# Optimization experiments

Hardware: AMD Instinct MI355X
Metric: run time of the kernel (lower is better)

## Reference

```python
import jax, jax.numpy as jnp
import numpy as np

D = 256; NH = 8; NL = 4; NP = 4; HD = D // NH
LEVELS = ((80, 80), (40, 40), (20, 20), (10, 10))
B = 8; LTXT = 32
LVIS = sum(h * w for h, w in LEVELS)  # 8500


def layer_norm(x, g, b):
    m = x.mean(-1, keepdims=True)
    v = ((x - m) ** 2).mean(-1, keepdims=True)
    return (x - m) * jax.lax.rsqrt(v + 1e-5) * g + b


def gelu(x):
    return jax.nn.gelu(x, approximate=False)


def sample_level(v, H, W, loc):
    # v: [B,NH,H*W,HD] level value; loc: [B,Lq,NH,NP,2] normalized [0,1] (x,y)
    # bilinear, align_corners=False, zero padding (matches grid_sample in MSDeformAttn)
    x = loc[..., 0] * W - 0.5
    y = loc[..., 1] * H - 0.5
    x0 = jnp.floor(x); y0 = jnp.floor(y)
    fx = x - x0; fy = y - y0
    Bq, Lq = loc.shape[0], loc.shape[1]
    out = jnp.zeros((Bq, NH, Lq * NP, HD), v.dtype)
    for dx in (0, 1):
        for dy in (0, 1):
            xi = x0 + dx; yi = y0 + dy
            w = (fx if dx else 1.0 - fx) * (fy if dy else 1.0 - fy)
            valid = (xi >= 0) & (xi < W) & (yi >= 0) & (yi < H)
            xi_c = jnp.clip(xi, 0, W - 1).astype(jnp.int32)
            yi_c = jnp.clip(yi, 0, H - 1).astype(jnp.int32)
            idx = (yi_c * W + xi_c).transpose(0, 2, 1, 3).reshape(Bq, NH, Lq * NP)
            wv = jnp.where(valid, w, 0.0).transpose(0, 2, 1, 3).reshape(Bq, NH, Lq * NP, 1)
            g = jnp.take_along_axis(v, idx[..., None], axis=2)  # [B,NH,Lq*NP,HD]
            out = out + g * wv
    return out.reshape(Bq, NH, Lq, NP, HD)


def setup_inputs() -> dict:
    key = jax.random.key(0)
    ks = iter(jax.random.split(key, 64))
    def rn(shape, s=1.0):
        return jax.random.normal(next(ks), shape, jnp.float32) * s
    inp = {}
    inp['txt_tokens'] = rn((B, LTXT, D))
    inp['vis_tokens'] = rn((B, LVIS, D))
    for i, (H, W) in enumerate(LEVELS):
        inp[f'feat{i}'] = rn((B, D, H, W))
    inp['spatial_shapes'] = jnp.array(LEVELS, jnp.int32)
    starts = np.cumsum([0] + [h * w for h, w in LEVELS])[:NL]
    inp['level_start_index'] = jnp.array(starts, jnp.int32)
    inp['reference_points'] = jax.random.uniform(next(ks), (B, LTXT, NL, 2), jnp.float32)
    inp['txt_pos'] = rn((B, LTXT, D), 0.02)
    inp['vis_pos'] = rn((B, LVIS, D), 0.02)
    s = 0.02
    # MSDeformAttn params
    inp['W_off'] = rn((D, NH * NL * NP * 2), s); inp['b_off'] = rn((NH * NL * NP * 2,), s)
    inp['W_aw'] = rn((D, NH * NL * NP), s); inp['b_aw'] = rn((NH * NL * NP,), s)
    inp['W_v'] = rn((D, D), s); inp['b_v'] = rn((D,), s)
    inp['W_do'] = rn((D, D), s); inp['b_do'] = rn((D,), s)
    # adapter projections
    inp['W_q_lvi'] = rn((D, D), s); inp['b_q_lvi'] = rn((D,), s)
    inp['W_out_lvi'] = rn((D, D), s); inp['b_out_lvi'] = rn((D,), s)
    # lvi norms + ffn
    inp['ln1_g'] = jnp.ones((D,)); inp['ln1_b'] = jnp.zeros((D,))
    inp['ln2_g'] = jnp.ones((D,)); inp['ln2_b'] = jnp.zeros((D,))
    inp['ffn1_W1'] = rn((D, 4 * D), s); inp['ffn1_b1'] = rn((4 * D,), s)
    inp['ffn1_W2'] = rn((4 * D, D), s); inp['ffn1_b2'] = rn((D,), s)
    # vli MultiheadAttention
    inp['Wq_m'] = rn((D, D), s); inp['bq_m'] = rn((D,), s)
    inp['Wk_m'] = rn((D, D), s); inp['bk_m'] = rn((D,), s)
    inp['Wv_m'] = rn((D, D), s); inp['bv_m'] = rn((D,), s)
    inp['Wo_m'] = rn((D, D), s); inp['bo_m'] = rn((D,), s)
    inp['vln1_g'] = jnp.ones((D,)); inp['vln1_b'] = jnp.zeros((D,))
    inp['vln2_g'] = jnp.ones((D,)); inp['vln2_b'] = jnp.zeros((D,))
    inp['ffn2_W1'] = rn((D, 4 * D), s); inp['ffn2_b1'] = rn((4 * D,), s)
    inp['ffn2_W2'] = rn((4 * D, D), s); inp['ffn2_b2'] = rn((D,), s)
    return inp


def reference(txt_tokens, vis_tokens, feat0, feat1, feat2, feat3, reference_points, txt_pos, vis_pos,
              W_off, b_off, W_aw, b_aw, W_v, b_v, W_do, b_do,
              W_q_lvi, b_q_lvi, W_out_lvi, b_out_lvi,
              ln1_g, ln1_b, ln2_g, ln2_b,
              ffn1_W1, ffn1_b1, ffn1_W2, ffn1_b2,
              Wq_m, bq_m, Wk_m, bk_m, Wv_m, bv_m, Wo_m, bo_m,
              vln1_g, vln1_b, vln2_g, vln2_b,
              ffn2_W1, ffn2_b1, ffn2_W2, ffn2_b2,
              spatial_shapes, level_start_index):
    # ---- lvi: deformable multi-scale attention (txt queries sample vis features) ----
    txt_query = txt_tokens + txt_pos
    q = txt_query @ W_q_lvi + b_q_lvi
    feats = (feat0, feat1, feat2, feat3)
    value = jnp.concatenate([f.reshape(f.shape[0], D, -1).transpose(0, 2, 1) for f in feats], axis=1)
    v = (value @ W_v + b_v).reshape(B, LVIS, NH, HD)
    off = (q @ W_off + b_off).reshape(B, LTXT, NH, NL, NP, 2)
    aw = jax.nn.softmax((q @ W_aw + b_aw).reshape(B, LTXT, NH, NL * NP), axis=-1).reshape(B, LTXT, NH, NL, NP)
    normalizer = jnp.array([[w, h] for h, w in LEVELS], jnp.float32)  # (W,H) per level
    loc = reference_points[:, :, None, :, None, :] + off / normalizer[None, None, None, :, None, :]
    acc = jnp.zeros((B, NH, LTXT, HD), v.dtype)
    start = 0
    for l, (H, W) in enumerate(LEVELS):
        vl = v[:, start:start + H * W].transpose(0, 2, 1, 3)  # [B,NH,HW,HD]
        s = sample_level(vl, H, W, loc[:, :, :, l])           # [B,NH,Lq,NP,HD]
        awl = aw[:, :, :, l].transpose(0, 2, 1, 3)[..., None]  # [B,NH,Lq,NP,1]
        acc = acc + (s * awl).sum(3)
        start += H * W
    d_out = acc.transpose(0, 2, 1, 3).reshape(B, LTXT, D) @ W_do + b_do
    txt_attn = d_out @ W_out_lvi + b_out_lvi
    txt_res = layer_norm(txt_tokens + txt_attn, ln1_g, ln1_b)
    ff = gelu(txt_res @ ffn1_W1 + ffn1_b1) @ ffn1_W2 + ffn1_b2
    txt_res = layer_norm(txt_res + ff, ln2_g, ln2_b)
    # ---- vli: standard cross attention (vis queries attend txt) ----
    vis_query = vis_tokens + vis_pos
    vis_key = txt_res + txt_pos
    qh = (vis_query @ Wq_m + bq_m).reshape(B, LVIS, NH, HD)
    kh = (vis_key @ Wk_m + bk_m).reshape(B, LTXT, NH, HD)
    vh = (vis_key @ Wv_m + bv_m).reshape(B, LTXT, NH, HD)
    scores = jnp.einsum('bqhd,bkhd->bhqk', qh, kh) / np.float32(np.sqrt(HD))
    p = jax.nn.softmax(scores, axis=-1)
    mo = jnp.einsum('bhqk,bkhd->bqhd', p, vh).reshape(B, LVIS, D) @ Wo_m + bo_m
    vis_res = layer_norm(vis_tokens + mo, vln1_g, vln1_b)
    ff2 = gelu(vis_res @ ffn2_W1 + ffn2_b1) @ ffn2_W2 + ffn2_b2
    vis_res = layer_norm(vis_res + ff2, vln2_g, vln2_b)
    attn_weights = p.mean(axis=1)  # torch MHA averages over heads
    return (txt_res, vis_res, attn_weights)
```

## Files before the change

### kernel.cpp

```cpp
#include <hip/hip_runtime.h>
#include <cstddef>

#define DD   256
#define NHH  8
#define HDD  32
#define BB   8
#define LT   32
#define LV   8500

typedef unsigned short u16;
typedef unsigned int   u32;
typedef __attribute__((ext_vector_type(8))) short short8;
typedef __attribute__((ext_vector_type(8))) unsigned short ushort8;
typedef __attribute__((ext_vector_type(4))) float f32x4;

__device__ __forceinline__ float gelu_f(float x) {
  return 0.5f * x * (1.0f + erff(x * 0.70710678118654752440f));
}

__device__ __forceinline__ u16 f2bf(float x) {
  u32 u = __float_as_uint(x);
  u += 0x7FFFu + ((u >> 16) & 1u);
  return (u16)(u >> 16);
}
__device__ __forceinline__ float bf2f(u16 h) { return __uint_as_float((u32)h << 16); }

__device__ __forceinline__ void gload16(const u16* g, u16* l) {
  __builtin_amdgcn_global_load_lds(
      (const __attribute__((address_space(1))) void*)g,
      (__attribute__((address_space(3))) void*)l, 16, 0, 0);
}

enum { AM_PLAIN = 0, AM_ADD = 1, AM_FEAT = 2, AM_HI = 3, AM_SPLIT = 4 };
enum { EP_BIAS = 0, EP_GELU = 1, EP_ACC = 2 };

template<int BM, int BN, int TM, int TN, int AMODE, int EPI>
__launch_bounds__(256)
__global__ void gemm_k(const float* __restrict__ A0, const float* __restrict__ A1,
                       const float* __restrict__ Wt, const float* __restrict__ bias,
                       float* __restrict__ C, int M, int K, int ldw, int ldc)
{
  constexpr int BK = 16;
  __shared__ __align__(16) float As[BK][BM];
  __shared__ __align__(16) float Ws[BK][BN];
  const int tid  = threadIdx.x;
  const int row0 = blockIdx.x * BM;
  const int col0 = blockIdx.y * BN;
  const int tx = tid % (BN / TN);
  const int ty = tid / (BN / TN);
  float acc[TM][TN] = {};

  for (int k0 = 0; k0 < K; k0 += BK) {
    {
      constexpr int AU = BM * BK / 4;
      for (int u = tid; u < AU; u += 256) {
        int m  = u / (BK / 4);
        int kq = (u % (BK / 4)) * 4;
        int grow = row0 + m;
        float4 v = make_float4(0.f, 0.f, 0.f, 0.f);
        if (grow < M) {
          v = *(const float4*)(A0 + (size_t)grow * K + k0 + kq);
          if constexpr (AMODE == AM_ADD) {
            float4 w = *(const float4*)(A1 + (size_t)grow * K + k0 + kq);
            v.x += w.x; v.y += w.y; v.z += w.z; v.w += w.w;
          }
        }
        As[kq + 0][m] = v.x; As[kq + 1][m] = v.y;
        As[kq + 2][m] = v.z; As[kq + 3][m] = v.w;
      }
    }
    {
      constexpr int WU = BK * BN / 4;
      for (int u = tid; u < WU; u += 256) {
        int k  = u / (BN / 4);
        int n4 = (u % (BN / 4)) * 4;
        *(float4*)&Ws[k][n4] =
            *(const float4*)(Wt + (size_t)(k0 + k) * ldw + col0 + n4);
      }
    }
    __syncthreads();

    #pragma unroll
    for (int k = 0; k < BK; ++k) {
      float a[TM], bv[TN];
      #pragma unroll
      for (int i = 0; i < TM; ++i) a[i] = As[k][ty * TM + i];
      #pragma unroll
      for (int j = 0; j < TN; j += 4) {
        float4 t4 = *(const float4*)&Ws[k][tx * TN + j];
        bv[j] = t4.x; bv[j + 1] = t4.y; bv[j + 2] = t4.z; bv[j + 3] = t4.w;
      }
      #pragma unroll
      for (int i = 0; i < TM; ++i)
        #pragma unroll
        for (int j = 0; j < TN; ++j)
          acc[i][j] = fmaf(a[i], bv[j], acc[i][j]);
    }
    __syncthreads();
  }

  #pragma unroll
  for (int i = 0; i < TM; ++i) {
    int r = row0 + ty * TM + i;
    if (r >= M) continue;
    #pragma unroll
    for (int j4 = 0; j4 < TN; j4 += 4) {
      int c = col0 + tx * TN + j4;
      float4 v = make_float4(acc[i][j4], acc[i][j4 + 1], acc[i][j4 + 2], acc[i][j4 + 3]);
      float4 b4 = *(const float4*)(bias + c);
      v.x += b4.x; v.y += b4.y; v.z += b4.z; v.w += b4.w;
      if constexpr (EPI == EP_GELU) {
        v.x = gelu_f(v.x); v.y = gelu_f(v.y); v.z = gelu_f(v.z); v.w = gelu_f(v.w);
      }
      *(float4*)(C + (size_t)r * ldc + c) = v;
    }
  }
}

__global__ void wsplit_kernel(const float* __restrict__ W, u16* __restrict__ hi,
                              u16* __restrict__ lo, int total, int Nw)
{
  int id = blockIdx.x * 256 + threadIdx.x;
  if (id >= total) return;
  int k = id / Nw, n = id - k * Nw;
  float x = W[id];
  u16 h = f2bf(x);
  u16 l = f2bf(x - bf2f(h));
  int o = ((k >> 3) * Nw + n) * 8 + (k & 7);
  hi[o] = h; lo[o] = l;
}

template<int AMODE, int EPI>
__global__ __launch_bounds__(256) void mgemm(
    const void* __restrict__ Ap, const void* __restrict__ A1p,
    const u16* __restrict__ Whi, const u16* __restrict__ Wlo,
    const float* __restrict__ bias, void* __restrict__ Cp,
    int M, int K, int lda, int ldc, int Nw, int wcol0, int ks0,
    const float* __restrict__ f0, const float* __restrict__ f1,
    const float* __restrict__ f2, const float* __restrict__ f3)
{
  constexpr bool GL = (AMODE >= 3);
  constexpr int SMEM_U16 = GL ? (AMODE == AM_SPLIT ? 16384 : 8192) : 8256;
  __shared__ __align__(16) u16 smem[SMEM_U16];
  const int tid  = threadIdx.x;
  const int lane = tid & 63;
  const int w    = tid >> 6;
  const int wr   = w >> 1, wc = w & 1;
  const int row0  = blockIdx.x * 128;
  const int colC0 = blockIdx.y * 128;
  f32x4 acc[4][4] = {};
  const int nk = K >> 5;

  if constexpr (GL) {
    const u16* Ah = (const u16*)Ap;
    const u16* Al = (const u16*)A1p;
    auto stage = [&](int t, int buf) {
      #pragma unroll
      for (int p = 0; p < 2; ++p) {
        int i = w + p * 4;
        int r = row0 + i * 16 + (lane >> 2);
        if (r >= M) r = M - 1;
        size_t goff = (size_t)r * lda + t * 32 + (lane & 3) * 8;
        gload16(Ah + goff, &smem[buf * 4096 + i * 512]);
        if constexpr (AMODE == AM_SPLIT)
          gload16(Al + goff, &smem[8192 + buf * 4096 + i * 512]);
      }
    };
    stage(0, 0);
    __syncthreads();
    for (int kt = 0; kt < nk; ++kt) {
      const int cur = kt & 1;
      if (kt + 1 < nk) stage(kt + 1, cur ^ 1);
      const int slot = lane >> 4;
      const int lrow = lane & 15;
      short8 ah[4], al[4], bh[4], bl[4];
      #pragma unroll
      for (int m = 0; m < 4; ++m) {
        int off = cur * 4096 + (((wr * 64 + m * 16 + lrow) << 2) + slot) * 8;
        ah[m] = *(const short8*)&smem[off];
        if constexpr (AMODE == AM_SPLIT) al[m] = *(const short8*)&smem[8192 + off];
      }
      #pragma unroll
      for (int n = 0; n < 4; ++n) {
        size_t off = ((size_t)((ks0 + kt) * 4 + slot) * Nw + wcol0 + colC0 + wc * 64 + n * 16 + lrow) * 8;
        bh[n] = *(const short8*)(Whi + off);
        bl[n] = *(const short8*)(Wlo + off);
      }
      #pragma unroll
      for (int m = 0; m < 4; ++m)
        #pragma unroll
        for (int n = 0; n < 4; ++n) {
          acc[m][n] = __builtin_amdgcn_mfma_f32_16x16x32_bf16(ah[m], bh[n], acc[m][n], 0, 0, 0);
          acc[m][n] = __builtin_amdgcn_mfma_f32_16x16x32_bf16(ah[m], bl[n], acc[m][n], 0, 0, 0);
          if constexpr (AMODE == AM_SPLIT)
            acc[m][n] = __builtin_amdgcn_mfma_f32_16x16x32_bf16(al[m], bh[n], acc[m][n], 0, 0, 0);
        }
      __syncthreads();
    }
  } else {
    u16* Ahi = smem;
    u16* Alo = smem + 4128;
    for (int kt = 0; kt < nk; ++kt) {
      #pragma unroll
      for (int p = 0; p < 4; ++p) {
        int j = tid + p * 256;
        int row, f4;
        if constexpr (AMODE == AM_FEAT) { f4 = j >> 7; row = j & 127; }
        else                            { row = j >> 3; f4 = j & 7; }
        int gr = row0 + row;
        float4 v = make_float4(0.f, 0.f, 0.f, 0.f);
        if (gr < M) {
          if constexpr (AMODE == AM_FEAT) {
            int b = gr / LV;
            int s = gr - b * LV;
            int l = (s >= 8400) ? 3 : (s >= 8000) ? 2 : (s >= 6400) ? 1 : 0;
            const float* fp = (l == 0) ? f0 : (l == 1) ? f1 : (l == 2) ? f2 : f3;
            const int hw = (l == 0) ? 6400 : (l == 1) ? 1600 : (l == 2) ? 400 : 100;
            const int st = (l == 0) ? 0 : (l == 1) ? 6400 : (l == 2) ? 8000 : 8400;
            const float* base = fp + ((size_t)b * DD + (kt * 32 + f4 * 4)) * hw + (s - st);
            v.x = base[0];
            v.y = base[(size_t)hw];
            v.z = base[2 * (size_t)hw];
            v.w = base[3 * (size_t)hw];
          } else {
            const float* Af = (const float*)Ap;
            v = *(const float4*)(Af + (size_t)gr * lda + kt * 32 + f4 * 4);
            if constexpr (AMODE == AM_ADD) {
              float4 u2 = *(const float4*)((const float*)A1p + (size_t)gr * lda + kt * 32 + f4 * 4);
              v.x += u2.x; v.y += u2.y; v.z += u2.z; v.w += u2.w;
            }
          }
        }
        int slot = f4 >> 1, half = f4 & 1;
        int off = (slot * 129 + row) * 8 + half * 4;
        u16 h0 = f2bf(v.x), h1 = f2bf(v.y), h2 = f2bf(v.z), h3 = f2bf(v.w);
        uint2 hp; hp.x = (u32)h0 | ((u32)h1 << 16); hp.y = (u32)h2 | ((u32)h3 << 16);
        *(uint2*)&Ahi[off] = hp;
        u16 l0 = f2bf(v.x - bf2f(h0)), l1 = f2bf(v.y - bf2f(h1));
        u16 l2 = f2bf(v.z - bf2f(h2)), l3 = f2bf(v.w - bf2f(h3));
        uint2 lp; lp.x = (u32)l0 | ((u32)l1 << 16); lp.y = (u32)l2 | ((u32)l3 << 16);
        *(uint2*)&Alo[off] = lp;
      }
      __syncthreads();

      const int slot = lane >> 4;
      const int lrow = lane & 15;
      short8 ah[4], al[4], bh[4], bl[4];
      #pragma unroll
      for (int m = 0; m < 4; ++m) {
        int off = (slot * 129 + wr * 64 + m * 16 + lrow) * 8;
        ah[m] = *(const short8*)&Ahi[off];
        al[m] = *(const short8*)&Alo[off];
      }
      #pragma unroll
      for (int n = 0; n < 4; ++n) {
        size_t off = ((size_t)((ks0 + kt) * 4 + slot) * Nw + wcol0 + colC0 + wc * 64 + n * 16 + lrow) * 8;
        bh[n] = *(const short8*)(Whi + off);
        bl[n] = *(const short8*)(Wlo + off);
      }
      #pragma unroll
      for (int m = 0; m < 4; ++m)
        #pragma unroll
        for (int n = 0; n < 4; ++n) {
          acc[m][n] = __builtin_amdgcn_mfma_f32_16x16x32_bf16(ah[m], bh[n], acc[m][n], 0, 0, 0);
          acc[m][n] = __builtin_amdgcn_mfma_f32_16x16x32_bf16(ah[m], bl[n], acc[m][n], 0, 0, 0);
          acc[m][n] = __builtin_amdgcn_mfma_f32_16x16x32_bf16(al[m], bh[n], acc[m][n], 0, 0, 0);
        }
      __syncthreads();
    }
  }

  const int lrow = lane & 15;
  #pragma unroll
  for (int m = 0; m < 4; ++m) {
    #pragma unroll
    for (int j = 0; j < 4; ++j) {
      int r = row0 + wr * 64 + m * 16 + ((lane >> 4) << 2) + j;
      if (r >= M) continue;
      #pragma unroll
      for (int n = 0; n < 4; ++n) {
        int c = colC0 + wc * 64 + n * 16 + lrow;
        float v = acc[m][n][j];
        if constexpr (EPI == EP_BIAS) {
          ((float*)Cp)[(size_t)r * ldc + c] = v + bias[c];
        } else if constexpr (EPI == EP_GELU) {
          ((u16*)Cp)[(size_t)r * ldc + c] = f2bf(gelu_f(v + bias[c]));
        } else {
          ((float*)Cp)[(size_t)r * ldc + c] += v;
        }
      }
    }
  }
}

__device__ __forceinline__ float4 ln_core(float4 x, const float* g, const float* bta, int lane) {
  float s  = x.x + x.y + x.z + x.w;
  float s2 = x.x * x.x + x.y * x.y + x.z * x.z + x.w * x.w;
  #pragma unroll
  for (int m = 1; m < 64; m <<= 1) {
    s  += __shfl_xor(s, m);
    s2 += __shfl_xor(s2, m);
  }
  float mean = s * (1.0f / 256.0f);
  float var  = s2 * (1.0f / 256.0f) - mean * mean;
  float rstd = rsqrtf(var + 1e-5f);
  float4 gg = *(const float4*)(g + lane * 4);
  float4 bb = *(const float4*)(bta + lane * 4);
  float4 o;
  o.x = (x.x - mean) * rstd * gg.x + bb.x;
  o.y = (x.y - mean) * rstd * gg.y + bb.y;
  o.z = (x.z - mean) * rstd * gg.z + bb.z;
  o.w = (x.w - mean) * rstd * gg.w + bb.w;
  return o;
}

__global__ void ln_kernel(const float* __restrict__ X, const float* __restrict__ R,
                          const float* __restrict__ g, const float* __restrict__ bta,
                          float* __restrict__ O, int M)
{
  int row  = blockIdx.x * 4 + (threadIdx.x >> 6);
  int lane = threadIdx.x & 63;
  if (row >= M) return;
  size_t base = (size_t)row * DD + lane * 4;
  float4 x = *(const float4*)(X + base);
  float4 r = *(const float4*)(R + base);
  x.x += r.x; x.y += r.y; x.z += r.z; x.w += r.w;
  float4 o = ln_core(x, g, bta, lane);
  *(float4*)(O + base) = o;
}

__global__ void ln_vis1(const float* __restrict__ X, const float* __restrict__ R,
                        const float* __restrict__ g, const float* __restrict__ bta,
                        u16* __restrict__ Oh, u16* __restrict__ Ol, int M)
{
  int row  = blockIdx.x * 4 + (threadIdx.x >> 6);
  int lane = threadIdx.x & 63;
  if (row >= M) return;
  size_t base = (size_t)row * DD + lane * 4;
  float4 x = *(const float4*)(X + base);
  float4 r = *(const float4*)(R + base);
  x.x += r.x; x.y += r.y; x.z += r.z; x.w += r.w;
  float4 o = ln_core(x, g, bta, lane);
  u16 h0 = f2bf(o.x), h1 = f2bf(o.y), h2 = f2bf(o.z), h3 = f2bf(o.w);
  uint2 hp; hp.x = (u32)h0 | ((u32)h1 << 16); hp.y = (u32)h2 | ((u32)h3 << 16);
  *(uint2*)(Oh + base) = hp;
  u16 l0 = f2bf(o.x - bf2f(h0)), l1 = f2bf(o.y - bf2f(h1));
  u16 l2 = f2bf(o.z - bf2f(h2)), l3 = f2bf(o.w - bf2f(h3));
  uint2 lp; lp.x = (u32)l0 | ((u32)l1 << 16); lp.y = (u32)l2 | ((u32)l3 << 16);
  *(uint2*)(Ol + base) = lp;
}

__global__ void ln_vis2(const float* __restrict__ X, const u16* __restrict__ Rh,
                        const u16* __restrict__ Rl, const float* __restrict__ g,
                        const float* __restrict__ bta, float* __restrict__ O, int M)
{
  int row  = blockIdx.x * 4 + (threadIdx.x >> 6);
  int lane = threadIdx.x & 63;
  if (row >= M) return;
  size_t base = (size_t)row * DD + lane * 4;
  float4 x = *(const float4*)(X + base);
  uint2 hp = *(const uint2*)(Rh + base);
  uint2 lp = *(const uint2*)(Rl + base);
  x.x += bf2f((u16)hp.x) + bf2f((u16)lp.x);
  x.y += bf2f((u16)(hp.x >> 16)) + bf2f((u16)(lp.x >> 16));
  x.z += bf2f((u16)hp.y) + bf2f((u16)lp.y);
  x.w += bf2f((u16)(hp.y >> 16)) + bf2f((u16)(lp.y >> 16));
  float4 o = ln_core(x, g, bta, lane);
  *(float4*)(O + base) = o;
}

__global__ void softloc_kernel(const float* __restrict__ awl, const float* __restrict__ offb,
                               const float* __restrict__ refp, float* __restrict__ aw,
                               float* __restrict__ loc)
{
  int idx = blockIdx.x * 256 + threadIdx.x;
  if (idx >= BB * LT * NHH) return;
  int h   = idx & 7;
  int row = idx >> 3;
  float v[16]; float mx = -1e30f;
  #pragma unroll
  for (int i = 0; i < 16; ++i) { v[i] = awl[row * 128 + h * 16 + i]; mx = fmaxf(mx, v[i]); }
  float sum = 0.f;
  #pragma unroll
  for (int i = 0; i < 16; ++i) { v[i] = expf(v[i] - mx); sum += v[i]; }
  float inv = 1.0f / sum;
  #pragma unroll
  for (int i = 0; i < 16; ++i) aw[row * 128 + h * 16 + i] = v[i] * inv;
  const float invn[4] = {1.f / 80.f, 1.f / 40.f, 1.f / 20.f, 1.f / 10.f};
  #pragma unroll
  for (int l = 0; l < 4; ++l) {
    float rx = refp[(row * 4 + l) * 2 + 0];
    float ry = refp[(row * 4 + l) * 2 + 1];
    #pragma unroll
    for (int p = 0; p < 4; ++p) {
      int o = row * 256 + h * 32 + l * 8 + p * 2;
      loc[o + 0] = rx + offb[o + 0] * invn[l];
      loc[o + 1] = ry + offb[o + 1] * invn[l];
    }
  }
}

__global__ void sampler_kernel(const float* __restrict__ vproj, const float* __restrict__ loc,
                               const float* __restrict__ aw, float* __restrict__ acc)
{
  int row = blockIdx.x;
  int t   = threadIdx.x;
  int h   = t >> 5, hd = t & 31;
  int b   = row >> 5;
  const float* vb = vproj + (size_t)b * LV * DD;
  const int Hs[4] = {80, 40, 20, 10};
  const int st[4] = {0, 6400, 8000, 8400};
  float a = 0.f;
  #pragma unroll
  for (int l = 0; l < 4; ++l) {
    const int Wl = Hs[l], Hl = Hs[l];
    #pragma unroll
    for (int p = 0; p < 4; ++p) {
      int o = row * 256 + h * 32 + l * 8 + p * 2;
      float lx  = loc[o + 0];
      float ly  = loc[o + 1];
      float wgt = aw[row * 128 + h * 16 + l * 4 + p];
      float x = lx * (float)Wl - 0.5f;
      float y = ly * (float)Hl - 0.5f;
      float x0f = floorf(x), y0f = floorf(y);
      float fx = x - x0f, fy = y - y0f;
      int x0 = (int)x0f, y0 = (int)y0f;
      #pragma unroll
      for (int dy = 0; dy < 2; ++dy) {
        #pragma unroll
        for (int dx = 0; dx < 2; ++dx) {
          int xi = x0 + dx, yi = y0 + dy;
          float w2 = (dx ? fx : 1.f - fx) * (dy ? fy : 1.f - fy);
          if (xi >= 0 && xi < Wl && yi >= 0 && yi < Hl) {
            a = fmaf(wgt * w2, vb[(size_t)(st[l] + yi * Wl + xi) * DD + h * 32 + hd], a);
          }
        }
      }
    }
  }
  acc[(size_t)row * DD + t] = a;
}

__global__ __launch_bounds__(512)
void attn_kernel(const float* __restrict__ qh, const float* __restrict__ kh,
                 const float* __restrict__ vh, u16* __restrict__ mo_hi,
                 u16* __restrict__ mo_lo, float* __restrict__ awout)
{
  const int b  = blockIdx.y;
  const int rl = threadIdx.x >> 5;
  const int l  = threadIdx.x & 31;
  const int h  = l >> 2;
  const int part = l & 3;
  const int s  = blockIdx.x * 16 + rl;
  if (s >= LV) return;
  const size_t row = (size_t)b * LV + s;
  const int c0 = h * 32 + part * 8;
  const float scale = 0.17677669529663687f;
  const float* Kb = kh + (size_t)b * 32 * DD;
  const float* Vb = vh + (size_t)b * 32 * DD;

  float q[8];
  {
    const float4* qp = (const float4*)(qh + row * DD + c0);
    float4 a = qp[0], c = qp[1];
    q[0]=a.x; q[1]=a.y; q[2]=a.z; q[3]=a.w; q[4]=c.x; q[5]=c.y; q[6]=c.z; q[7]=c.w;
  }

  float sc[32]; float mx = -1e30f;
  #pragma unroll
  for (int k = 0; k < 32; ++k) {
    const float4* kp = (const float4*)(Kb + k * DD + c0);
    float4 a = kp[0], c = kp[1];
    float d = 0.f;
    d = fmaf(q[0], a.x, d); d = fmaf(q[1], a.y, d); d = fmaf(q[2], a.z, d); d = fmaf(q[3], a.w, d);
    d = fmaf(q[4], c.x, d); d = fmaf(q[5], c.y, d); d = fmaf(q[6], c.z, d); d = fmaf(q[7], c.w, d);
    d += __shfl_xor(d, 1);
    d += __shfl_xor(d, 2);
    sc[k] = d * scale;
    mx = fmaxf(mx, sc[k]);
  }
  float sum = 0.f;
  #pragma unroll
  for (int k = 0; k < 32; ++k) { sc[k] = expf(sc[k] - mx); sum += sc[k]; }
  const float inv = 1.0f / sum;
  #pragma unroll
  for (int k = 0; k < 32; ++k) sc[k] *= inv;

  float o[8] = {};
  #pragma unroll
  for (int k = 0; k < 32; ++k) {
    const float4* vp = (const float4*)(Vb + k * DD + c0);
    float4 a = vp[0], c = vp[1];
    const float pk = sc[k];
    o[0] = fmaf(pk, a.x, o[0]); o[1] = fmaf(pk, a.y, o[1]);
    o[2] = fmaf(pk, a.z, o[2]); o[3] = fmaf(pk, a.w, o[3]);
    o[4] = fmaf(pk, c.x, o[4]); o[5] = fmaf(pk, c.y, o[5]);
    o[6] = fmaf(pk, c.z, o[6]); o[7] = fmaf(pk, c.w, o[7]);
  }
  {
    u16 hh[8], ll[8];
    #pragma unroll
    for (int j = 0; j < 8; ++j) {
      hh[j] = f2bf(o[j]);
      ll[j] = f2bf(o[j] - bf2f(hh[j]));
    }
    uint4 hp, lp;
    hp.x = (u32)hh[0] | ((u32)hh[1] << 16); hp.y = (u32)hh[2] | ((u32)hh[3] << 16);
    hp.z = (u32)hh[4] | ((u32)hh[5] << 16); hp.w = (u32)hh[6] | ((u32)hh[7] << 16);
    lp.x = (u32)ll[0] | ((u32)ll[1] << 16); lp.y = (u32)ll[2] | ((u32)ll[3] << 16);
    lp.z = (u32)ll[4] | ((u32)ll[5] << 16); lp.w = (u32)ll[6] | ((u32)ll[7] << 16);
    *(uint4*)(mo_hi + row * DD + c0) = hp;
    *(uint4*)(mo_lo + row * DD + c0) = lp;
  }
  #pragma unroll
  for (int k = 0; k < 32; ++k) {
    float v = sc[k];
    v += __shfl_xor(v, 4);
    v += __shfl_xor(v, 8);
    v += __shfl_xor(v, 16);
    if (h == 0 && (k >> 3) == part) awout[row * 32 + k] = v * 0.125f;
  }
}

extern "C" void kernel_launch(void* const* d_in, const int* in_sizes, int n_in,
                              void* d_out, int out_size, void* d_ws, size_t ws_size,
                              hipStream_t stream)
{
  const float* txt_tokens = (const float*)d_in[0];
  const float* vis_tokens = (const float*)d_in[1];
  const float* feat0 = (const float*)d_in[2];
  const float* feat1 = (const float*)d_in[3];
  const float* feat2 = (const float*)d_in[4];
  const float* feat3 = (const float*)d_in[5];
  const float* refp    = (const float*)d_in[8];
  const float* txt_pos = (const float*)d_in[9];
  const float* vis_pos = (const float*)d_in[10];
  const float* W_off = (const float*)d_in[11]; const float* b_off = (const float*)d_in[12];
  const float* W_aw  = (const float*)d_in[13]; const float* b_aw  = (const float*)d_in[14];
  const float* W_v   = (const float*)d_in[15]; const float* b_v   = (const float*)d_in[16];
  const float* W_do  = (const float*)d_in[17]; const float* b_do  = (const float*)d_in[18];
  const float* W_q   = (const float*)d_in[19]; const float* b_q   = (const float*)d_in[20];
  const float* W_out = (const float*)d_in[21]; const float* b_out = (const float*)d_in[22];
  const float* ln1_g = (const float*)d_in[23]; const float* ln1_b = (const float*)d_in[24];
  const float* ln2_g = (const float*)d_in[25]; const float* ln2_b = (const float*)d_in[26];
  const float* f1W1  = (const float*)d_in[27]; const float* f1b1  = (const float*)d_in[28];
  const float* f1W2  = (const float*)d_in[29]; const float* f1b2  = (const float*)d_in[30];
  const float* Wq_m  = (const float*)d_in[31]; const float* bq_m  = (const float*)d_in[32];
  const float* Wk_m  = (const float*)d_in[33]; const float* bk_m  = (const float*)d_in[34];
  const float* Wv_m  = (const float*)d_in[35]; const float* bv_m  = (const float*)d_in[36];
  const float* Wo_m  = (const float*)d_in[37]; const float* bo_m  = (const float*)d_in[38];
  const float* vln1_g = (const float*)d_in[39]; const float* vln1_b = (const float*)d_in[40];
  const float* vln2_g = (const float*)d_in[41]; const float* vln2_b = (const float*)d_in[42];
  const float* f2W1  = (const float*)d_in[43]; const float* f2b1  = (const float*)d_in[44];
  const float* f2W2  = (const float*)d_in[45]; const float* f2b2  = (const float*)d_in[46];

  const int MV = BB * LV;
  float* ws = (float*)d_ws;
  const size_t BIG = (size_t)MV * DD;
  float* buf0 = ws;
  float* buf1 = ws + BIG;
  float* buf2 = ws + 2 * BIG;
  float* sm   = ws + 3 * BIG;
  float* qb    = sm;
  float* offb  = qb + 65536;
  float* awlb  = offb + 65536;
  float* awb   = awlb + 32768;
  float* locb  = awb + 32768;
  float* accb  = locb + 65536;
  float* doutb = accb + 65536;
  float* tattn = doutb + 65536;
  float* tres1 = tattn + 65536;
  float* ffh   = tres1 + 65536;
  float* ffb   = ffh + 262144;
  float* khb   = ffb + 65536;
  float* vhb   = khb + 65536;
  u16* wsp   = (u16*)(vhb + 65536);
  u16* wv_hi = wsp;               u16* wv_lo = wv_hi + 65536;
  u16* wq_hi = wv_lo + 65536;     u16* wq_lo = wq_hi + 65536;
  u16* wo_hi = wq_lo + 65536;     u16* wo_lo = wo_hi + 65536;
  u16* w1_hi = wo_lo + 65536;     u16* w1_lo = w1_hi + 262144;
  u16* w2_hi = w1_lo + 262144;    u16* w2_lo = w2_hi + 262144;

  u16* mo_hi = (u16*)buf2;  u16* mo_lo = mo_hi + BIG;
  u16* ln_hi = (u16*)buf1;  u16* ln_lo = ln_hi + BIG;
  u16* hid   = (u16*)buf2;

  float* out_txt = (float*)d_out;
  float* out_vis = out_txt + (size_t)BB * LT * DD;
  float* out_aw  = out_vis + BIG;

  dim3 blk(256);
  #define NOF nullptr, nullptr, nullptr, nullptr

  wsplit_kernel<<<256, blk, 0, stream>>>(W_v,  wv_hi, wv_lo, 65536, 256);
  wsplit_kernel<<<256, blk, 0, stream>>>(Wq_m, wq_hi, wq_lo, 65536, 256);
  wsplit_kernel<<<256, blk, 0, stream>>>(Wo_m, wo_hi, wo_lo, 65536, 256);
  wsplit_kernel<<<1024, blk, 0, stream>>>(f2W1, w1_hi, w1_lo, 262144, 1024);
  wsplit_kernel<<<1024, blk, 0, stream>>>(f2W2, w2_hi, w2_lo, 262144, 256);

  mgemm<AM_FEAT, EP_BIAS><<<dim3(532, 2), blk, 0, stream>>>(
      nullptr, nullptr, wv_hi, wv_lo, b_v, buf0, MV, DD, DD, DD, DD, 0, 0,
      feat0, feat1, feat2, feat3);
  mgemm<AM_ADD, EP_BIAS><<<dim3(532, 2), blk, 0, stream>>>(
      vis_tokens, vis_pos, wq_hi, wq_lo, bq_m, buf1, MV, DD, DD, DD, DD, 0, 0, NOF);

  gemm_k<32,64,2,4,AM_ADD,EP_BIAS><<<dim3(8,4), blk, 0, stream>>>(
      txt_tokens, txt_pos, W_q, b_q, qb, 256, DD, DD, DD);
  gemm_k<32,64,2,4,AM_PLAIN,EP_BIAS><<<dim3(8,4), blk, 0, stream>>>(
      qb, nullptr, W_off, b_off, offb, 256, DD, DD, DD);
  gemm_k<32,64,2,4,AM_PLAIN,EP_BIAS><<<dim3(8,2), blk, 0, stream>>>(
      qb, nullptr, W_aw, b_aw, awlb, 256, DD, 128, 128);
  softloc_kernel<<<8, blk, 0, stream>>>(awlb, offb, refp, awb, locb);
  sampler_kernel<<<256, blk, 0, stream>>>(buf0, locb, awb, accb);
  gemm_k<32,64,2,4,AM_PLAIN,EP_BIAS><<<dim3(8,4), blk, 0, stream>>>(
      accb, nullptr, W_do, b_do, doutb, 256, DD, DD, DD);
  gemm_k<32,64,2,4,AM_PLAIN,EP_BIAS><<<dim3(8,4), blk, 0, stream>>>(
      doutb, nullptr, W_out, b_out, tattn, 256, DD, DD, DD);
  ln_kernel<<<64, blk, 0, stream>>>(tattn, txt_tokens, ln1_g, ln1_b, tres1, 256);
  gemm_k<32,64,2,4,AM_PLAIN,EP_GELU><<<dim3(8,16), blk, 0, stream>>>(
      tres1, nullptr, f1W1, f1b1, ffh, 256, DD, 1024, 1024);
  gemm_k<32,64,2,4,AM_PLAIN,EP_BIAS><<<dim3(8,4), blk, 0, stream>>>(
      ffh, nullptr, f1W2, f1b2, ffb, 256, 1024, DD, DD);
  ln_kernel<<<64, blk, 0, stream>>>(ffb, tres1, ln2_g, ln2_b, out_txt, 256);

  gemm_k<32,64,2,4,AM_ADD,EP_BIAS><<<dim3(8,4), blk, 0, stream>>>(
      out_txt, txt_pos, Wk_m, bk_m, khb, 256, DD, DD, DD);
  gemm_k<32,64,2,4,AM_ADD,EP_BIAS><<<dim3(8,4), blk, 0, stream>>>(
      out_txt, txt_pos, Wv_m, bv_m, vhb, 256, DD, DD, DD);

  attn_kernel<<<dim3(532, 8), dim3(512), 0, stream>>>(buf1, khb, vhb, mo_hi, mo_lo, out_aw);
  mgemm<AM_SPLIT, EP_BIAS><<<dim3(532, 2), blk, 0, stream>>>(
      mo_hi, mo_lo, wo_hi, wo_lo, bo_m, buf0, MV, DD, 256, DD, DD, 0, 0, NOF);
  ln_vis1<<<17000, blk, 0, stream>>>(buf0, vis_tokens, vln1_g, vln1_b, ln_hi, ln_lo, MV);

  for (int c = 0; c < 2; ++c) {
    mgemm<AM_SPLIT, EP_GELU><<<dim3(532, 4), blk, 0, stream>>>(
        ln_hi, ln_lo, w1_hi, w1_lo, f2b1 + c * 512, hid,
        MV, DD, 256, 512, 1024, c * 512, 0, NOF);
    if (c == 0) {
      mgemm<AM_HI, EP_BIAS><<<dim3(532, 2), blk, 0, stream>>>(
          hid, nullptr, w2_hi, w2_lo, f2b2, buf0,
          MV, 512, 512, DD, DD, 0, 0, NOF);
    } else {
      mgemm<AM_HI, EP_ACC><<<dim3(532, 2), blk, 0, stream>>>(
          hid, nullptr, w2_hi, w2_lo, nullptr, buf0,
          MV, 512, 512, DD, DD, 0, 16, NOF);
    }
  }
  ln_vis2<<<17000, blk, 0, stream>>>(buf0, ln_hi, ln_lo, vln2_g, vln2_b, out_vis, MV);
  #undef NOF
}
```

Before: 1.288 ms.

## Merge FFN2 chunks into single GEMMs, stage attention K/V in LDS, fuse weight splits

The two-chunk FFN2 loop, with its read-modify-write accumulation, becomes one W1 GEMM that writes the GELU hidden halves into two buffers. A single K=1024 W2 GEMM then reads both halves and writes directly into the output buffer, which removes extra launches and the accumulate pass. The attention kernel now loads per-batch K/V into shared memory instead of reading them repeatedly from global memory. The five weight-split launches are merged into one. The risks are shared-memory pressure in the 512-thread attention kernel and that running ln_vis2 in place on out_vis depends on it reading each row before writing it.

```diff
diff --git a/kernel.cpp b/kernel.cpp
--- a/kernel.cpp
+++ b/kernel.cpp
@@ -117,13 +117,25 @@
   }
 }
 
-__global__ void wsplit_kernel(const float* __restrict__ W, u16* __restrict__ hi,
-                              u16* __restrict__ lo, int total, int Nw)
+__global__ void wsplit_all(const float* __restrict__ Wv, const float* __restrict__ Wq,
+                           const float* __restrict__ Wo, const float* __restrict__ W1,
+                           const float* __restrict__ W2,
+                           u16* __restrict__ wv_hi, u16* __restrict__ wv_lo,
+                           u16* __restrict__ wq_hi, u16* __restrict__ wq_lo,
+                           u16* __restrict__ wo_hi, u16* __restrict__ wo_lo,
+                           u16* __restrict__ w1_hi, u16* __restrict__ w1_lo,
+                           u16* __restrict__ w2_hi, u16* __restrict__ w2_lo)
 {
   int id = blockIdx.x * 256 + threadIdx.x;
-  if (id >= total) return;
-  int k = id / Nw, n = id - k * Nw;
-  float x = W[id];
+  const float* W; u16 *hi, *lo; int Nw, lid;
+  if (id < 65536)       { W = Wv; hi = wv_hi; lo = wv_lo; Nw = 256;  lid = id; }
+  else if (id < 131072) { W = Wq; hi = wq_hi; lo = wq_lo; Nw = 256;  lid = id - 65536; }
+  else if (id < 196608) { W = Wo; hi = wo_hi; lo = wo_lo; Nw = 256;  lid = id - 131072; }
+  else if (id < 458752) { W = W1; hi = w1_hi; lo = w1_lo; Nw = 1024; lid = id - 196608; }
+  else if (id < 720896) { W = W2; hi = w2_hi; lo = w2_lo; Nw = 256;  lid = id - 458752; }
+  else return;
+  int k = lid / Nw, n = lid - k * Nw;
+  float x = W[lid];
   u16 h = f2bf(x);
   u16 l = f2bf(x - bf2f(h));
   int o = ((k >> 3) * Nw + n) * 8 + (k & 7);
@@ -134,7 +146,7 @@
 __global__ __launch_bounds__(256) void mgemm(
     const void* __restrict__ Ap, const void* __restrict__ A1p,
     const u16* __restrict__ Whi, const u16* __restrict__ Wlo,
-    const float* __restrict__ bias, void* __restrict__ Cp,
+    const float* __restrict__ bias, void* __restrict__ Cp, void* __restrict__ Cp2,
     int M, int K, int lda, int ldc, int Nw, int wcol0, int ks0,
     const float* __restrict__ f0, const float* __restrict__ f1,
     const float* __restrict__ f2, const float* __restrict__ f3)
@@ -154,14 +166,19 @@
   if constexpr (GL) {
     const u16* Ah = (const u16*)Ap;
     const u16* Al = (const u16*)A1p;
+    const int half = nk >> 1;
     auto stage = [&](int t, int buf) {
+      const u16* base = Ah; int t2 = t;
+      if constexpr (AMODE == AM_HI) {
+        if (Al != nullptr && t >= half) { base = Al; t2 = t - half; }
+      }
       #pragma unroll
       for (int p = 0; p < 2; ++p) {
         int i = w + p * 4;
         int r = row0 + i * 16 + (lane >> 2);
         if (r >= M) r = M - 1;
-        size_t goff = (size_t)r * lda + t * 32 + (lane & 3) * 8;
-        gload16(Ah + goff, &smem[buf * 4096 + i * 512]);
+        size_t goff = (size_t)r * lda + t2 * 32 + (lane & 3) * 8;
+        gload16(base + goff, &smem[buf * 4096 + i * 512]);
         if constexpr (AMODE == AM_SPLIT)
           gload16(Al + goff, &smem[8192 + buf * 4096 + i * 512]);
       }
@@ -231,8 +248,8 @@
             }
           }
         }
-        int slot = f4 >> 1, half = f4 & 1;
-        int off = (slot * 129 + row) * 8 + half * 4;
+        int slot = f4 >> 1, half2 = f4 & 1;
+        int off = (slot * 129 + row) * 8 + half2 * 4;
         u16 h0 = f2bf(v.x), h1 = f2bf(v.y), h2 = f2bf(v.z), h3 = f2bf(v.w);
         uint2 hp; hp.x = (u32)h0 | ((u32)h1 << 16); hp.y = (u32)h2 | ((u32)h3 << 16);
         *(uint2*)&Ahi[off] = hp;
@@ -284,7 +301,8 @@
         if constexpr (EPI == EP_BIAS) {
           ((float*)Cp)[(size_t)r * ldc + c] = v + bias[c];
         } else if constexpr (EPI == EP_GELU) {
-          ((u16*)Cp)[(size_t)r * ldc + c] = f2bf(gelu_f(v + bias[c]));
+          u16* dst = (u16*)((c < ldc) ? Cp : Cp2);
+          dst[(size_t)r * ldc + (c & (ldc - 1))] = f2bf(gelu_f(v + bias[c]));
         } else {
           ((float*)Cp)[(size_t)r * ldc + c] += v;
         }
@@ -446,7 +464,21 @@
                  const float* __restrict__ vh, u16* __restrict__ mo_hi,
                  u16* __restrict__ mo_lo, float* __restrict__ awout)
 {
-  const int b  = blockIdx.y;
+  __shared__ __align__(16) float4 Ks[2048];
+  __shared__ __align__(16) float4 Vs[2048];
+  const int b = blockIdx.y;
+  {
+    const float4* ksrc = (const float4*)(kh + (size_t)b * 32 * DD);
+    const float4* vsrc = (const float4*)(vh + (size_t)b * 32 * DD);
+    for (int u = threadIdx.x; u < 2048; u += 512) {
+      int k = u >> 6, c = u & 63;
+      int slot = (k * 2 + (c & 1)) * 32 + (c >> 1);
+      Ks[slot] = ksrc[u];
+      Vs[slot] = vsrc[u];
+    }
+  }
+  __syncthreads();
+
   const int rl = threadIdx.x >> 5;
   const int l  = threadIdx.x & 31;
   const int h  = l >> 2;
@@ -456,8 +488,6 @@
   const size_t row = (size_t)b * LV + s;
   const int c0 = h * 32 + part * 8;
   const float scale = 0.17677669529663687f;
-  const float* Kb = kh + (size_t)b * 32 * DD;
-  const float* Vb = vh + (size_t)b * 32 * DD;
 
   float q[8];
   {
@@ -469,8 +499,8 @@
   float sc[32]; float mx = -1e30f;
   #pragma unroll
   for (int k = 0; k < 32; ++k) {
-    const float4* kp = (const float4*)(Kb + k * DD + c0);
-    float4 a = kp[0], c = kp[1];
+    float4 a = Ks[(k * 2 + 0) * 32 + l];
+    float4 c = Ks[(k * 2 + 1) * 32 + l];
     float d = 0.f;
     d = fmaf(q[0], a.x, d); d = fmaf(q[1], a.y, d); d = fmaf(q[2], a.z, d); d = fmaf(q[3], a.w, d);
     d = fmaf(q[4], c.x, d); d = fmaf(q[5], c.y, d); d = fmaf(q[6], c.z, d); d = fmaf(q[7], c.w, d);
@@ -489,8 +519,8 @@
   float o[8] = {};
   #pragma unroll
   for (int k = 0; k < 32; ++k) {
-    const float4* vp = (const float4*)(Vb + k * DD + c0);
-    float4 a = vp[0], c = vp[1];
+    float4 a = Vs[(k * 2 + 0) * 32 + l];
+    float4 c = Vs[(k * 2 + 1) * 32 + l];
     const float pk = sc[k];
     o[0] = fmaf(pk, a.x, o[0]); o[1] = fmaf(pk, a.y, o[1]);
     o[2] = fmaf(pk, a.z, o[2]); o[3] = fmaf(pk, a.w, o[3]);
@@ -583,7 +613,8 @@
 
   u16* mo_hi = (u16*)buf2;  u16* mo_lo = mo_hi + BIG;
   u16* ln_hi = (u16*)buf1;  u16* ln_lo = ln_hi + BIG;
-  u16* hid   = (u16*)buf2;
+  u16* hidA  = (u16*)buf2;
+  u16* hidB  = (u16*)buf0;
 
   float* out_txt = (float*)d_out;
   float* out_vis = out_txt + (size_t)BB * LT * DD;
@@ -592,17 +623,14 @@
   dim3 blk(256);
   #define NOF nullptr, nullptr, nullptr, nullptr
 
-  wsplit_kernel<<<256, blk, 0, stream>>>(W_v,  wv_hi, wv_lo, 65536, 256);
-  wsplit_kernel<<<256, blk, 0, stream>>>(Wq_m, wq_hi, wq_lo, 65536, 256);
-  wsplit_kernel<<<256, blk, 0, stream>>>(Wo_m, wo_hi, wo_lo, 65536, 256);
-  wsplit_kernel<<<1024, blk, 0, stream>>>(f2W1, w1_hi, w1_lo, 262144, 1024);
-  wsplit_kernel<<<1024, blk, 0, stream>>>(f2W2, w2_hi, w2_lo, 262144, 256);
+  wsplit_all<<<2816, blk, 0, stream>>>(W_v, Wq_m, Wo_m, f2W1, f2W2,
+      wv_hi, wv_lo, wq_hi, wq_lo, wo_hi, wo_lo, w1_hi, w1_lo, w2_hi, w2_lo);
 
   mgemm<AM_FEAT, EP_BIAS><<<dim3(532, 2), blk, 0, stream>>>(
-      nullptr, nullptr, wv_hi, wv_lo, b_v, buf0, MV, DD, DD, DD, DD, 0, 0,
+      nullptr, nullptr, wv_hi, wv_lo, b_v, buf0, nullptr, MV, DD, DD, DD, DD, 0, 0,
       feat0, feat1, feat2, feat3);
   mgemm<AM_ADD, EP_BIAS><<<dim3(532, 2), blk, 0, stream>>>(
-      vis_tokens, vis_pos, wq_hi, wq_lo, bq_m, buf1, MV, DD, DD, DD, DD, 0, 0, NOF);
+      vis_tokens, vis_pos, wq_hi, wq_lo, bq_m, buf1, nullptr, MV, DD, DD, DD, DD, 0, 0, NOF);
 
   gemm_k<32,64,2,4,AM_ADD,EP_BIAS><<<dim3(8,4), blk, 0, stream>>>(
       txt_tokens, txt_pos, W_q, b_q, qb, 256, DD, DD, DD);
@@ -630,23 +658,15 @@
 
   attn_kernel<<<dim3(532, 8), dim3(512), 0, stream>>>(buf1, khb, vhb, mo_hi, mo_lo, out_aw);
   mgemm<AM_SPLIT, EP_BIAS><<<dim3(532, 2), blk, 0, stream>>>(
-      mo_hi, mo_lo, wo_hi, wo_lo, bo_m, buf0, MV, DD, 256, DD, DD, 0, 0, NOF);
+      mo_hi, mo_lo, wo_hi, wo_lo, bo_m, buf0, nullptr, MV, DD, 256, DD, DD, 0, 0, NOF);
   ln_vis1<<<17000, blk, 0, stream>>>(buf0, vis_tokens, vln1_g, vln1_b, ln_hi, ln_lo, MV);
 
-  for (int c = 0; c < 2; ++c) {
-    mgemm<AM_SPLIT, EP_GELU><<<dim3(532, 4), blk, 0, stream>>>(
-        ln_hi, ln_lo, w1_hi, w1_lo, f2b1 + c * 512, hid,
-        MV, DD, 256, 512, 1024, c * 512, 0, NOF);
-    if (c == 0) {
-      mgemm<AM_HI, EP_BIAS><<<dim3(532, 2), blk, 0, stream>>>(
-          hid, nullptr, w2_hi, w2_lo, f2b2, buf0,
-          MV, 512, 512, DD, DD, 0, 0, NOF);
-    } else {
-      mgemm<AM_HI, EP_ACC><<<dim3(532, 2), blk, 0, stream>>>(
-          hid, nullptr, w2_hi, w2_lo, nullptr, buf0,
-          MV, 512, 512, DD, DD, 0, 16, NOF);
-    }
-  }
-  ln_vis2<<<17000, blk, 0, stream>>>(buf0, ln_hi, ln_lo, vln2_g, vln2_b, out_vis, MV);
+  mgemm<AM_SPLIT, EP_GELU><<<dim3(532, 8), blk, 0, stream>>>(
+      ln_hi, ln_lo, w1_hi, w1_lo, f2b1, hidA, hidB,
+      MV, DD, 256, 512, 1024, 0, 0, NOF);
+  mgemm<AM_HI, EP_BIAS><<<dim3(532, 2), blk, 0, stream>>>(
+      hidA, hidB, w2_hi, w2_lo, f2b2, out_vis, nullptr,
+      MV, 1024, 512, DD, DD, 0, 0, NOF);
+  ln_vis2<<<17000, blk, 0, stream>>>(out_vis, ln_hi, ln_lo, vln2_g, vln2_b, out_vis, MV);
   #undef NOF
 }
```

After: 1.183 ms. 8.2% less time.
